# Performance work log

Measured on AMD Instinct MI355X. Metric: run time of the kernel, lower is better.

## Reference

```python
import jax, jax.numpy as jnp
from jax import lax
import numpy as np

B, C, L = 32, 8, 512
C_IN = 512      # must equal L (tokenConv consumes permuted tensor)
D_MODEL = 512
SCALE_NUM = 64  # 63 actual scales


def build_wavelet_bank(scale_num, LB=-8.0, UB=8.0, N=1024, Fb=2.0, Fc=8.0):
    """Replicates cmor_torch; returns centered zero-padded kernel bank [S, K].
    Zero-centering is exact because every kernel length (16*s+1) is odd and K is odd,
    so the padded conv with pad=(K-1)//2 equals the original per-scale conv with
    pad=(k-1)//2."""
    x = np.linspace(LB, UB, N)
    wav = (np.pi * Fb) ** (-0.5) * np.exp(2j * np.pi * Fc * x) * np.exp(-x ** 2 / Fb)
    step = x[1] - x[0]
    kernels = []
    for scale in np.arange(1, scale_num):
        j = (np.arange(scale * (x[-1] - x[0]) + 1) / (scale * step)).astype(int)
        j = j[j < wav.size]
        kernels.append(np.real(wav[j]) * scale ** (-0.5))
    K = max(len(k) for k in kernels)
    if K % 2 == 0:
        K += 1
    bank = np.zeros((len(kernels), K), np.float32)
    for i, k in enumerate(kernels):
        assert (K - len(k)) % 2 == 0, "kernel parity mismatch"
        off = (K - len(k)) // 2
        bank[i, off:off + len(k)] = k
    return bank


def setup_inputs() -> dict:
    key = jax.random.key(0)
    k1, k2 = jax.random.split(key)
    x = jax.random.normal(k1, (B, C, L), dtype=jnp.float32)
    wavelet_bank = jnp.asarray(build_wavelet_bank(SCALE_NUM))  # [63, K]
    token_w = jax.random.normal(k2, (D_MODEL, C_IN, 3), dtype=jnp.float32) * 0.02
    return {"x": x, "wavelet_bank": wavelet_bank, "token_w": token_w}


def reference(x, wavelet_bank, token_w):
    Bb, Cc, Ll = x.shape
    S, K = wavelet_bank.shape
    pad = (K - 1) // 2
    # fused CWT over all (channel, scale) pairs: [B*C, 1, L] conv [S, 1, K] -> [B*C, S, L]
    xr = x.reshape(Bb * Cc, 1, Ll)
    conv = lax.conv_general_dilated(
        xr, wavelet_bank[:, None, :], window_strides=(1,),
        padding=[(pad, pad)], dimension_numbers=("NCH", "OIH", "NCH"))
    d = jnp.abs(jnp.diff(conv, axis=-1))                 # [B*C, S, L-1]
    d = jnp.concatenate([d, d[..., -1:]], axis=-1)       # replicate last sample -> L
    feats = d.reshape(Bb, Cc * S, Ll)
    out = jnp.concatenate([x, feats], axis=1)            # [B, C*(1+S), L]
    # tokenConv on permuted tensor: channels = L (= c_in), length = C*(1+S)
    h = out.transpose(0, 2, 1)                           # [B, L, C_total]
    hp = jnp.concatenate([h[..., -1:], h, h[..., :1]], axis=-1)  # circular pad=1
    y = lax.conv_general_dilated(
        hp, token_w, window_strides=(1,), padding="VALID",
        dimension_numbers=("NCH", "OIH", "NCH"))         # [B, d_model, C_total]
    return y.transpose(0, 2, 1)                          # [B, C_total, d_model]
```

## Files before the change

### kernel.cpp

```cpp
#include <hip/hip_runtime.h>
#include <hip/hip_bf16.h>

#define NB 32
#define NC 8
#define NL 512
#define NS 63
#define NK 1009
#define NPAD 504
#define ND 512
#define NCT 512
#define NROWS 514

typedef __attribute__((ext_vector_type(4))) float f32x4;
typedef __attribute__((ext_vector_type(8))) short short8;
typedef __attribute__((ext_vector_type(4))) short short4v;

#define APAD_BYTES (NB * NROWS * NL * 2)
#define WB_BYTES   (3 * ND * NL * 2)
#define BANKB_BYTES (64 * 1024 * 2)

typedef const __attribute__((address_space(1))) unsigned int* gp1_t;
typedef __attribute__((address_space(3))) unsigned int* lp3_t;
__device__ __forceinline__ void gload_lds16(const void* g, void* l) {
  __builtin_amdgcn_global_load_lds((gp1_t)g, (lp3_t)l, 16, 0, 0);
}

__device__ __forceinline__ unsigned short bf16_bits(float v) {
  return __builtin_bit_cast(unsigned short, __float2bfloat16(v));
}

#define WAITVM(N) asm volatile("s_waitcnt vmcnt(" #N ")" ::: "memory")
#define FENCE() asm volatile("" ::: "memory")
#define BAR() __builtin_amdgcn_s_barrier()

__global__ __launch_bounds__(256) void prep_kernel(
    const float* __restrict__ bank, const float* __restrict__ tw,
    __hip_bfloat16* __restrict__ Wb, __hip_bfloat16* __restrict__ bankB) {
  const int idx = blockIdx.x * 256 + threadIdx.x;

  {
    int i0 = idx * 4;
    const float4* t4 = (const float4*)(tw + (size_t)i0 * 3);
    float4 a = t4[0], bq = t4[1], c4 = t4[2];
    ushort4 w0 = make_ushort4(bf16_bits(a.x), bf16_bits(a.w), bf16_bits(bq.z), bf16_bits(c4.y));
    ushort4 w1 = make_ushort4(bf16_bits(a.y), bf16_bits(bq.x), bf16_bits(bq.w), bf16_bits(c4.z));
    ushort4 w2 = make_ushort4(bf16_bits(a.z), bf16_bits(bq.y), bf16_bits(c4.x), bf16_bits(c4.w));
    *(ushort4*)(Wb + 0 * ND * NL + i0) = w0;
    *(ushort4*)(Wb + 1 * ND * NL + i0) = w1;
    *(ushort4*)(Wb + 2 * ND * NL + i0) = w2;
  }
  {
    int s = idx >> 10, k = idx & 1023;
    float v = (s < NS && k < NK) ? bank[s * NK + k] : 0.f;
    bankB[idx] = __float2bfloat16(v);
  }
}

#define CPY_STRIDE 3088

__global__ __launch_bounds__(512) void cwt_kernel(
    const float* __restrict__ x, const __hip_bfloat16* __restrict__ bankB,
    __hip_bfloat16* __restrict__ Apad) {
  __shared__ char smem[8 * 8192 + 4 * CPY_STRIDE];
  char* bankS = smem;
  char* cpy = smem + 8 * 8192;

  const int tid = threadIdx.x;
  const int gid = blockIdx.x;
  const int bc = gid >> 1, h = gid & 1;
  const int b = bc >> 3, c = bc & 7;
  const int w = tid >> 6, l = tid & 63;
  const int hi = l >> 4, li = l & 15;
  const int ma = h ? 1 : 0, mb = h ? 2 : 3;

  const float* xrow = x + bc * NL;

  if (h == 0) {
    __hip_bfloat16 v = __float2bfloat16(xrow[tid & 511]);
    if (tid < 512) {
      Apad[((size_t)(b * NROWS) + 1 + c) * NL + tid] = v;
      if (c == 0) Apad[((size_t)(b * NROWS) + 513) * NL + tid] = v;
    }
  }

  for (int i = 0; i < 6; ++i) {
    int p = tid + i * 512;
    int r_ = p / 768, pe = p - r_ * 768;
    int e0 = 2 * pe;
    int i0 = e0 + r_;
    float xa = (i0 >= NPAD && i0 < NPAD + NL) ? xrow[i0 - NPAD] : 0.f;
    float xb = (i0 + 1 >= NPAD && i0 + 1 < NPAD + NL) ? xrow[i0 + 1 - NPAD] : 0.f;
    float xc = (i0 + 2 >= NPAD && i0 + 2 < NPAD + NL) ? xrow[i0 + 2 - NPAD] : 0.f;
    unsigned short u0 = bf16_bits(xb - xa);
    unsigned short u1 = bf16_bits(xc - xb);
    *(unsigned int*)(cpy + r_ * CPY_STRIDE + e0 * 2) = (unsigned)u0 | ((unsigned)u1 << 16);
  }

#define STAGE(kt)                                                             \
  {                                                                           \
    int s_ = tid >> 4, rb = tid & 15;                                         \
    int j = (s_ < 16) ? (ma * 16 + s_) : (mb * 16 + (s_ - 16));               \
    int srcc = rb ^ (s_ & 7);                                                 \
    gload_lds16(bankB + j * 1024 + (kt) * 128 + srcc * 8,                     \
                bankS + (kt) * 8192 + tid * 16);                              \
  }

#define CCOMP(kt, A0, A1)                                                      \
  {                                                                            \
    _Pragma("unroll") for (int ksl = 0; ksl < 4; ++ksl) {                      \
      short8 bv[4];                                                            \
      _Pragma("unroll") for (int n = 0; n < 4; ++n) {                          \
        int t = tbase + n * 16 + li;                                           \
        int e = t - r + (kt) * 128 + ksl * 32 + hi * 8;                        \
        const char* pc = cpy + r * CPY_STRIDE + e * 2;                         \
        short4v lo = *(const short4v*)pc;                                      \
        short4v hh = *(const short4v*)(pc + 8);                                \
        short8 f;                                                              \
        f[0] = lo[0]; f[1] = lo[1]; f[2] = lo[2]; f[3] = lo[3];                \
        f[4] = hh[0]; f[5] = hh[1]; f[6] = hh[2]; f[7] = hh[3];                \
        bv[n] = f;                                                             \
      }                                                                        \
      if (A0) {                                                                \
        int lrow = li;                                                         \
        int chunk = (ksl * 4 + hi) ^ (lrow & 7);                               \
        short8 av = *(const short8*)(bankS + (kt) * 8192 + lrow * 256 + chunk * 16); \
        _Pragma("unroll") for (int n = 0; n < 4; ++n)                          \
          acc[0][n] = __builtin_amdgcn_mfma_f32_16x16x32_bf16(av, bv[n],       \
                                                              acc[0][n], 0, 0, 0); \
      }                                                                        \
      if (A1) {                                                                \
        int lrow = 16 + li;                                                    \
        int chunk = (ksl * 4 + hi) ^ (lrow & 7);                               \
        short8 av = *(const short8*)(bankS + (kt) * 8192 + lrow * 256 + chunk * 16); \
        _Pragma("unroll") for (int n = 0; n < 4; ++n)                          \
          acc[1][n] = __builtin_amdgcn_mfma_f32_16x16x32_bf16(av, bv[n],       \
                                                              acc[1][n], 0, 0, 0); \
      }                                                                        \
    }                                                                          \
  }

  f32x4 acc[2][4] = {};
  const int r = l & 3;
  const int tbase = w * 64;

  if (h == 0) {
    STAGE(0); STAGE(1); STAGE(2); STAGE(3);
    STAGE(4); STAGE(5); STAGE(6); STAGE(7);
    asm volatile("s_waitcnt vmcnt(7) lgkmcnt(0)" ::: "memory");
    BAR(); FENCE(); CCOMP(0, 0, 1);
    WAITVM(6); BAR(); FENCE(); CCOMP(1, 0, 1);
    WAITVM(5); BAR(); FENCE(); CCOMP(2, 1, 1);
    WAITVM(4); BAR(); FENCE(); CCOMP(3, 1, 1);
    WAITVM(3); BAR(); FENCE(); CCOMP(4, 1, 1);
    WAITVM(2); BAR(); FENCE(); CCOMP(5, 0, 1);
    WAITVM(1); BAR(); FENCE(); CCOMP(6, 0, 1);
    WAITVM(0); BAR(); FENCE(); CCOMP(7, 0, 1);
  } else {
    STAGE(0); STAGE(1); STAGE(2); STAGE(3);
    STAGE(4); STAGE(5); STAGE(6);
    asm volatile("s_waitcnt vmcnt(6) lgkmcnt(0)" ::: "memory");
    BAR(); FENCE(); CCOMP(0, 0, 1);
    WAITVM(5); BAR(); FENCE(); CCOMP(1, 1, 1);
    WAITVM(4); BAR(); FENCE(); CCOMP(2, 1, 1);
    WAITVM(3); BAR(); FENCE(); CCOMP(3, 1, 1);
    WAITVM(2); BAR(); FENCE(); CCOMP(4, 1, 1);
    WAITVM(1); BAR(); FENCE(); CCOMP(5, 1, 1);
    WAITVM(0); BAR(); FENCE(); CCOMP(6, 0, 1);
  }

#pragma unroll
  for (int mm = 0; mm < 2; ++mm) {
    const int mblk = mm ? mb : ma;
#pragma unroll
    for (int rg = 0; rg < 4; ++rg) {
      int jg = mblk * 16 + hi * 4 + rg;
      if (jg >= NS) continue;
      int ch = 8 + c * NS + jg;
      size_t rowbase = ((size_t)(b * NROWS) + 1 + ch) * NL;
#pragma unroll
      for (int n = 0; n < 4; ++n) {
        int t = tbase + n * 16 + li;
        float d = fabsf(acc[mm][n][rg]);
        __hip_bfloat16 hv = __float2bfloat16(d);
        bool lastgrp = (w == 7 && n == 3);
        bool skip = lastgrp && (li == 15);
        bool dup = lastgrp && (li == 14);
        if (!skip) Apad[rowbase + t] = hv;
        if (dup) Apad[rowbase + 511] = hv;
        if (ch == NCT - 1) {
          size_t wrapbase = (size_t)(b * NROWS) * NL;
          if (!skip) Apad[wrapbase + t] = hv;
          if (dup) Apad[wrapbase + 511] = hv;
        }
      }
    }
  }
#undef STAGE
#undef CCOMP
}

__global__ __launch_bounds__(256) void gemm_kernel(
    const __hip_bfloat16* __restrict__ Ap, const __hip_bfloat16* __restrict__ Wb,
    float* __restrict__ out) {
  __shared__ char sAr[2 * 8192];
  __shared__ char sBr[2 * 24576];
  __shared__ char bnd[2048];
  __shared__ char dump[2048];

  const int tid = threadIdx.x;
  const int gid = blockIdx.x;
  const int q = gid >> 3;
  const int pid = (gid & 7) * 16 + (q >> 2);
  const int b = pid >> 2;
  const int p0 = (pid & 3) * 128;
  const int o0 = (q & 3) * 128;

  const int w = tid >> 6, lane = tid & 63;
  const int wm = w >> 1, wn = w & 1;
  const int row_in = lane & 15, hi = lane >> 4;

  const int rA0 = tid >> 2, cgA0 = (tid & 3) ^ ((rA0 >> 1) & 3);
  const int ck1 = tid + 256;
  const int rA1 = ck1 >> 2, cgA1 = (ck1 & 3) ^ ((rA1 >> 1) & 3);

  {
    int r_ = (tid >> 6) & 1;
    int col = tid & 63;
    const __hip_bfloat16* src =
        Ap + ((size_t)(b * NROWS) + p0 + 128 + r_) * NL + col * 8;
    char* dst = (tid < 128) ? (bnd + tid * 16) : (dump + (tid - 128) * 16);
    gload_lds16(src, dst);
  }

#define GSTAGE(kk, bu)                                                         \
  {                                                                            \
    const int l0_ = (kk) * 32;                                                 \
    gload_lds16(Ap + ((b * NROWS + p0 + rA0) * NL + l0_ + cgA0 * 8),           \
                sAr + (bu) * 8192 + tid * 16);                                 \
    gload_lds16(Ap + ((b * NROWS + p0 + rA1) * NL + l0_ + cgA1 * 8),           \
                sAr + (bu) * 8192 + ck1 * 16);                                 \
    _Pragma("unroll") for (int g = 0; g < 6; ++g) {                            \
      int id = g * 256 + tid;                                                  \
      int kap_ = id >> 9, ckb = id & 511;                                      \
      int row = ckb >> 2, cg = (ckb & 3) ^ ((row >> 1) & 3);                   \
      gload_lds16(Wb + ((kap_ * ND + o0 + row) * NL + l0_ + cg * 8),           \
                  sBr + (bu) * 24576 + id * 16);                               \
    }                                                                          \
  }

#define COMPUTE(bu, kk)                                                        \
  {                                                                            \
    const int l0_ = (kk) * 32;                                                 \
    _Pragma("unroll") for (int kap_ = 0; kap_ < 3; ++kap_) {                   \
      short8 av[4], bv[4];                                                     \
      _Pragma("unroll") for (int m = 0; m < 4; ++m) {                          \
        int arow = wm * 64 + m * 16 + row_in + kap_;                           \
        const char* pa;                                                        \
        if (m == 3) {                                                          \
          pa = (arow < 128)                                                    \
             ? (sAr + (bu) * 8192 + (arow * 4 + (hi ^ ((arow >> 1) & 3))) * 16)\
             : (bnd + (arow - 128) * 1024 + (l0_ + hi * 8) * 2);               \
        } else {                                                               \
          pa = sAr + (bu) * 8192 + (arow * 4 + (hi ^ ((arow >> 1) & 3))) * 16; \
        }                                                                      \
        av[m] = *(const short8*)pa;                                            \
      }                                                                        \
      _Pragma("unroll") for (int n = 0; n < 4; ++n) {                          \
        int brow = wn * 64 + n * 16 + row_in;                                  \
        bv[n] = *(const short8*)(sBr + (bu) * 24576 + kap_ * 8192 +            \
                                 (brow * 4 + (hi ^ ((brow >> 1) & 3))) * 16);  \
      }                                                                        \
      _Pragma("unroll") for (int m = 0; m < 4; ++m)                            \
        _Pragma("unroll") for (int n = 0; n < 4; ++n)                          \
          acc[m][n] = __builtin_amdgcn_mfma_f32_16x16x32_bf16(av[m], bv[n],    \
                                                              acc[m][n], 0, 0, 0); \
    }                                                                          \
  }

  f32x4 acc[4][4] = {};

  GSTAGE(0, 0);

  for (int kk = 0; kk < 15; ++kk) {
    GSTAGE(kk + 1, (kk + 1) & 1);
    WAITVM(8);
    BAR(); FENCE();
    COMPUTE(kk & 1, kk);
    FENCE(); BAR();
  }
  WAITVM(0); BAR(); FENCE();
  COMPUTE(1, 15);
#undef GSTAGE
#undef COMPUTE

#pragma unroll
  for (int m = 0; m < 4; ++m) {
    const int p = p0 + wm * 64 + m * 16 + hi * 4;
#pragma unroll
    for (int n = 0; n < 4; ++n) {
      const int o = o0 + wn * 64 + n * 16 + row_in;
#pragma unroll
      for (int r = 0; r < 4; ++r)
        out[(size_t)((b * NCT) + p + r) * ND + o] = acc[m][n][r];
    }
  }
}

extern "C" void kernel_launch(void* const* d_in, const int* in_sizes, int n_in,
                              void* d_out, int out_size, void* d_ws, size_t ws_size,
                              hipStream_t stream) {
  const float* x = (const float*)d_in[0];
  const float* bank = (const float*)d_in[1];
  const float* tw = (const float*)d_in[2];
  float* out = (float*)d_out;

  char* ws = (char*)d_ws;
  __hip_bfloat16* Apad = (__hip_bfloat16*)ws;
  __hip_bfloat16* Wb = (__hip_bfloat16*)(ws + APAD_BYTES);
  __hip_bfloat16* bankB = (__hip_bfloat16*)(ws + APAD_BYTES + WB_BYTES);

  prep_kernel<<<256, 256, 0, stream>>>(bank, tw, Wb, bankB);
  cwt_kernel<<<512, 512, 0, stream>>>(x, bankB, Apad);
  gemm_kernel<<<512, 256, 0, stream>>>(Apad, Wb, out);
}
```

Measured before the change: 62.42 us.

## Load A fragments directly into registers and deepen B LDS pipeline

The GEMM no longer stages the A operand through LDS. Each wave loads its A fragments straight from global memory into registers, with register triple-buffering two steps ahead. B tiles are staged per (tap, k-chunk) through a 5-deep LDS ring with one barrier per step, so the K loop now runs 48 steps over the three taps instead of 16 steps with three taps each. This removes the LDS traffic and boundary-row handling for A and shrinks LDS use. In exchange it relies on uncoalesced direct global loads for A and on vmcnt accounting being correct across the deeper pipeline.

```diff
diff --git a/kernel.cpp b/kernel.cpp
--- a/kernel.cpp
+++ b/kernel.cpp
@@ -17,7 +17,6 @@
 
 #define APAD_BYTES (NB * NROWS * NL * 2)
 #define WB_BYTES   (3 * ND * NL * 2)
-#define BANKB_BYTES (64 * 1024 * 2)
 
 typedef const __attribute__((address_space(1))) unsigned int* gp1_t;
 typedef __attribute__((address_space(3))) unsigned int* lp3_t;
@@ -202,10 +201,7 @@
 __global__ __launch_bounds__(256) void gemm_kernel(
     const __hip_bfloat16* __restrict__ Ap, const __hip_bfloat16* __restrict__ Wb,
     float* __restrict__ out) {
-  __shared__ char sAr[2 * 8192];
-  __shared__ char sBr[2 * 24576];
-  __shared__ char bnd[2048];
-  __shared__ char dump[2048];
+  __shared__ __hip_bfloat16 sB[5][128 * 32];
 
   const int tid = threadIdx.x;
   const int gid = blockIdx.x;
@@ -219,79 +215,78 @@
   const int wm = w >> 1, wn = w & 1;
   const int row_in = lane & 15, hi = lane >> 4;
 
-  const int rA0 = tid >> 2, cgA0 = (tid & 3) ^ ((rA0 >> 1) & 3);
+  const int r0 = tid >> 2, cg0 = (tid & 3) ^ ((r0 >> 1) & 3);
   const int ck1 = tid + 256;
-  const int rA1 = ck1 >> 2, cgA1 = (ck1 & 3) ^ ((rA1 >> 1) & 3);
+  const int r1 = ck1 >> 2, cg1 = (ck1 & 3) ^ ((r1 >> 1) & 3);
+
+#define BSTAGE(kk, bu)                                                         \
+  {                                                                            \
+    const int kap_ = (kk) >> 4;                                                \
+    const int l0_ = ((kk) & 15) << 5;                                          \
+    gload_lds16(Wb + ((kap_ * ND + o0 + r0) * NL + l0_ + cg0 * 8),             \
+                &sB[bu][tid * 8]);                                             \
+    gload_lds16(Wb + ((kap_ * ND + o0 + r1) * NL + l0_ + cg1 * 8),             \
+                &sB[bu][ck1 * 8]);                                             \
+  }
+
+#define ALOAD(kk, AV)                                                          \
+  {                                                                            \
+    const int kap_ = (kk) >> 4;                                                \
+    const int l0_ = ((kk) & 15) << 5;                                          \
+    _Pragma("unroll") for (int m = 0; m < 4; ++m)                              \
+      AV[m] = *(const short8*)(Ap +                                            \
+          ((size_t)(b * NROWS) + p0 + kap_ + wm * 64 + m * 16 + row_in) * NL + \
+          l0_ + hi * 8);                                                       \
+  }
+
+#define COMPUTE(bu, AV)                                                        \
+  {                                                                            \
+    short8 bv[4];                                                              \
+    _Pragma("unroll") for (int n = 0; n < 4; ++n) {                            \
+      int row = wn * 64 + n * 16 + row_in;                                     \
+      int slot = row * 4 + (hi ^ ((row >> 1) & 3));                            \
+      bv[n] = *(const short8*)(&sB[bu][slot * 8]);                             \
+    }                                                                          \
+    _Pragma("unroll") for (int m = 0; m < 4; ++m)                              \
+      _Pragma("unroll") for (int n = 0; n < 4; ++n)                            \
+        acc[m][n] = __builtin_amdgcn_mfma_f32_16x16x32_bf16(AV[m], bv[n],      \
+                                                            acc[m][n], 0, 0, 0); \
+  }
+
+#define STEP(kk, CUR, NX, bu, bs)                                              \
+  ALOAD((kk) + 2, NX); FENCE();                                                \
+  BSTAGE((kk) + 3, bs);                                                        \
+  WAITVM(14); BAR(); FENCE();                                                  \
+  COMPUTE(bu, CUR); FENCE();
+
+  f32x4 acc[4][4] = {};
+  short8 avA[4], avB[4], avC[4];
+
+  ALOAD(0, avA); FENCE();
+  ALOAD(1, avB); FENCE();
+  BSTAGE(0, 0); BSTAGE(1, 1); BSTAGE(2, 2);
 
   {
-    int r_ = (tid >> 6) & 1;
-    int col = tid & 63;
-    const __hip_bfloat16* src =
-        Ap + ((size_t)(b * NROWS) + p0 + 128 + r_) * NL + col * 8;
-    char* dst = (tid < 128) ? (bnd + tid * 16) : (dump + (tid - 128) * 16);
-    gload_lds16(src, dst);
-  }
-
-#define GSTAGE(kk, bu)                                                         \
-  {                                                                            \
-    const int l0_ = (kk) * 32;                                                 \
-    gload_lds16(Ap + ((b * NROWS + p0 + rA0) * NL + l0_ + cgA0 * 8),           \
-                sAr + (bu) * 8192 + tid * 16);                                 \
-    gload_lds16(Ap + ((b * NROWS + p0 + rA1) * NL + l0_ + cgA1 * 8),           \
-                sAr + (bu) * 8192 + ck1 * 16);                                 \
-    _Pragma("unroll") for (int g = 0; g < 6; ++g) {                            \
-      int id = g * 256 + tid;                                                  \
-      int kap_ = id >> 9, ckb = id & 511;                                      \
-      int row = ckb >> 2, cg = (ckb & 3) ^ ((row >> 1) & 3);                   \
-      gload_lds16(Wb + ((kap_ * ND + o0 + row) * NL + l0_ + cg * 8),           \
-                  sBr + (bu) * 24576 + id * 16);                               \
-    }                                                                          \
-  }
-
-#define COMPUTE(bu, kk)                                                        \
-  {                                                                            \
-    const int l0_ = (kk) * 32;                                                 \
-    _Pragma("unroll") for (int kap_ = 0; kap_ < 3; ++kap_) {                   \
-      short8 av[4], bv[4];                                                     \
-      _Pragma("unroll") for (int m = 0; m < 4; ++m) {                          \
-        int arow = wm * 64 + m * 16 + row_in + kap_;                           \
-        const char* pa;                                                        \
-        if (m == 3) {                                                          \
-          pa = (arow < 128)                                                    \
-             ? (sAr + (bu) * 8192 + (arow * 4 + (hi ^ ((arow >> 1) & 3))) * 16)\
-             : (bnd + (arow - 128) * 1024 + (l0_ + hi * 8) * 2);               \
-        } else {                                                               \
-          pa = sAr + (bu) * 8192 + (arow * 4 + (hi ^ ((arow >> 1) & 3))) * 16; \
-        }                                                                      \
-        av[m] = *(const short8*)pa;                                            \
-      }                                                                        \
-      _Pragma("unroll") for (int n = 0; n < 4; ++n) {                          \
-        int brow = wn * 64 + n * 16 + row_in;                                  \
-        bv[n] = *(const short8*)(sBr + (bu) * 24576 + kap_ * 8192 +            \
-                                 (brow * 4 + (hi ^ ((brow >> 1) & 3))) * 16);  \
-      }                                                                        \
-      _Pragma("unroll") for (int m = 0; m < 4; ++m)                            \
-        _Pragma("unroll") for (int n = 0; n < 4; ++n)                          \
-          acc[m][n] = __builtin_amdgcn_mfma_f32_16x16x32_bf16(av[m], bv[n],    \
-                                                              acc[m][n], 0, 0, 0); \
-    }                                                                          \
-  }
-
-  f32x4 acc[4][4] = {};
-
-  GSTAGE(0, 0);
-
-  for (int kk = 0; kk < 15; ++kk) {
-    GSTAGE(kk + 1, (kk + 1) & 1);
-    WAITVM(8);
-    BAR(); FENCE();
-    COMPUTE(kk & 1, kk);
-    FENCE(); BAR();
-  }
-  WAITVM(0); BAR(); FENCE();
-  COMPUTE(1, 15);
-#undef GSTAGE
+    int bu = 0;
+    for (int g = 0; g < 15; ++g) {
+      const int kk = g * 3;
+      int bs = bu + 3; if (bs >= 5) bs -= 5;
+      STEP(kk + 0, avA, avC, bu, bs);
+      bu = (bu == 4) ? 0 : bu + 1; bs = bu + 3; if (bs >= 5) bs -= 5;
+      STEP(kk + 1, avB, avA, bu, bs);
+      bu = (bu == 4) ? 0 : bu + 1; bs = bu + 3; if (bs >= 5) bs -= 5;
+      STEP(kk + 2, avC, avB, bu, bs);
+      bu = (bu == 4) ? 0 : bu + 1;
+    }
+  }
+  ALOAD(47, avC); FENCE();
+  WAITVM(12); BAR(); FENCE(); COMPUTE(0, avA); FENCE();
+  WAITVM(6);  BAR(); FENCE(); COMPUTE(1, avB); FENCE();
+  WAITVM(0);  BAR(); FENCE(); COMPUTE(2, avC);
+#undef BSTAGE
+#undef ALOAD
 #undef COMPUTE
+#undef STEP
 
 #pragma unroll
   for (int m = 0; m < 4; ++m) {
```

After: 87.93 us. 40.9% more time.
